# Optimization experiments

Hardware: AMD Instinct MI355X
Metric: run time of the kernel (lower is better)

## Reference

```python
import jax, jax.numpy as jnp
import numpy as np

EPS = 1e-5
NEG_SLOPE = 0.01


def setup_inputs() -> dict:
    key = jax.random.key(0)
    ks = jax.random.split(key, 5)
    B, T, I, H = 16, 16384, 64, 128
    s = 1.0 / np.sqrt(H)
    return {
        "x": jax.random.normal(ks[0], (B, T, I), dtype=jnp.float32),
        "W_ih": jax.random.normal(ks[1], (4 * H, I), dtype=jnp.float32) * s,
        "W_hh": jax.random.normal(ks[2], (4 * H, H), dtype=jnp.float32) * s,
        "b_ih": jax.random.normal(ks[3], (4 * H,), dtype=jnp.float32) * s,
        "b_hh": jax.random.normal(ks[4], (4 * H,), dtype=jnp.float32) * s,
        "gamma": jnp.ones((H,), dtype=jnp.float32),
        "beta": jnp.zeros((H,), dtype=jnp.float32),
    }


def _lstm(x, W_ih, W_hh, b_ih, b_hh):
    B, T, _ = x.shape
    H = W_hh.shape[1]
    # Precompute input contributions for all timesteps: [B, T, 4H]
    gx = jnp.einsum('bti,gi->btg', x, W_ih) + b_ih + b_hh

    def step(carry, g_t):
        h, c = carry
        g = g_t + h @ W_hh.T  # [B, 4H]
        i, f, gg, o = jnp.split(g, 4, axis=-1)  # PyTorch gate order i,f,g,o
        i = jax.nn.sigmoid(i)
        f = jax.nn.sigmoid(f)
        gg = jnp.tanh(gg)
        o = jax.nn.sigmoid(o)
        c = f * c + i * gg
        h = o * jnp.tanh(c)
        return (h, c), h

    h0 = jnp.zeros((B, H), dtype=x.dtype)
    (hn, cn), out = jax.lax.scan(step, (h0, h0), jnp.swapaxes(gx, 0, 1))
    return jnp.swapaxes(out, 0, 1), hn, cn  # out: [B, T, H]


def reference(x, W_ih, W_hh, b_ih, b_hh, gamma, beta):
    B, T, _ = x.shape
    H = W_hh.shape[1]
    out, hn, cn = _lstm(x, W_ih, W_hh, b_ih, b_hh)
    # BatchNorm1d (training mode) over flattened [B*T, H]
    flat = out.reshape(-1, H)
    mean = flat.mean(axis=0)
    var = flat.var(axis=0)  # biased variance, as PyTorch uses for normalization
    norm = (flat - mean) * jax.lax.rsqrt(var + EPS) * gamma + beta
    y = jax.nn.leaky_relu(norm.reshape(B, T, H), NEG_SLOPE)
    return (y, (hn[None], cn[None]))  # hn/cn: [num_layers=1, B, H]
```

## Files before the change

### kernel.cpp

```cpp
#include <hip/hip_runtime.h>
#include <hip/hip_bf16.h>
#include <cstdint>

#define TB 16
#define TT 16384
#define TI 64
#define TH 128
#define TG 512

typedef _Float16 half2_t __attribute__((ext_vector_type(2)));

__device__ __forceinline__ float sigf(float z) {
    return 1.0f / (1.0f + __expf(-z));
}
__device__ __forceinline__ float tanhf_fast(float z) {
    return 2.0f / (1.0f + __expf(-2.0f * z)) - 1.0f;
}
__device__ __forceinline__ float4 ld4(const float* p) {
    return *reinterpret_cast<const float4*>(p);
}
__device__ __forceinline__ void fma4(float4& acc, const float4 w, const float4 h) {
    acc.x = fmaf(w.x, h.x, acc.x);
    acc.y = fmaf(w.y, h.y, acc.y);
    acc.z = fmaf(w.z, h.z, acc.z);
    acc.w = fmaf(w.w, h.w, acc.w);
}
__device__ __forceinline__ float hsum4(const float4 a) {
    return (a.x + a.y) + (a.z + a.w);
}
__device__ __forceinline__ void pin2(half2_t& v) {
    asm volatile("" : "+v"(v));
}

__global__ __launch_bounds__(256, 2) void gx_precompute(
    const float* __restrict__ x, const float* __restrict__ W_ih,
    const float* __restrict__ b_ih, const float* __restrict__ b_hh,
    float* __restrict__ gx)
{
    const int tid  = threadIdx.x;
    const int j    = tid & (TH - 1);
    const int pair = tid >> 7;
    const int row_a = pair * 2 * TH + j;
    const int row_b = row_a + TH;

    float4 ua[TI / 4], ub[TI / 4];
#pragma unroll
    for (int k4 = 0; k4 < TI / 4; ++k4) {
        ua[k4] = ld4(W_ih + (size_t)row_a * TI + k4 * 4);
        ub[k4] = ld4(W_ih + (size_t)row_b * TI + k4 * 4);
    }
    const float bias_a = b_ih[row_a] + b_hh[row_a];
    const float bias_b = b_ih[row_b] + b_hh[row_b];

    __shared__ __align__(16) float xs[2][TI];
    const int ROWS = 128;
    const size_t r0 = (size_t)blockIdx.x * ROWS;

    if (tid < TI / 4)
        *reinterpret_cast<float4*>(&xs[0][tid * 4]) = ld4(x + r0 * TI + tid * 4);
    __syncthreads();
    float4 xreg = make_float4(0.f, 0.f, 0.f, 0.f);
    if (tid < TI / 4) xreg = ld4(x + (r0 + 1) * TI + tid * 4);

#pragma unroll 1
    for (int rr = 0; rr < ROWS; ++rr) {
        const float* xrow = xs[rr & 1];
        float4 aa = make_float4(0.f, 0.f, 0.f, 0.f);
        float4 ab = make_float4(0.f, 0.f, 0.f, 0.f);
#pragma unroll
        for (int k4 = 0; k4 < TI / 4; ++k4) {
            const float4 x4 = *reinterpret_cast<const float4*>(&xrow[k4 * 4]);
            fma4(aa, ua[k4], x4);
            fma4(ab, ub[k4], x4);
        }
        if (tid < TI / 4) {
            if (rr + 1 < ROWS)
                *reinterpret_cast<float4*>(&xs[(rr + 1) & 1][tid * 4]) = xreg;
            if (rr + 2 < ROWS) xreg = ld4(x + (r0 + rr + 2) * TI + tid * 4);
        }
        float* grow = gx + (r0 + rr) * (size_t)TG;
        grow[row_a] = hsum4(aa) + bias_a;
        grow[row_b] = hsum4(ab) + bias_b;

        asm volatile("s_waitcnt lgkmcnt(0)" ::: "memory");
        __builtin_amdgcn_s_barrier();
    }
}

__global__
__attribute__((amdgpu_flat_work_group_size(512, 512), amdgpu_waves_per_eu(2, 2)))
void lstm_scan_fp16(
    const float* __restrict__ W_hh, const float* __restrict__ gx,
    float* __restrict__ y, float* __restrict__ hn, float* __restrict__ cn)
{
    const int b    = blockIdx.x;
    const int tid  = threadIdx.x;
    const int j    = tid & (TH - 1);
    const int gate = tid >> 7;

    __shared__ __align__(16) half2_t h2_lds[TH / 2];
    __shared__ __align__(16) float   g_lds[TG];

    half2_t wh2[TH / 2];
#pragma unroll
    for (int k = 0; k < TH / 4; ++k) {
        const float4 wv = ld4(W_hh + (size_t)tid * TH + k * 4);
        wh2[2 * k]     = half2_t{(_Float16)wv.x, (_Float16)wv.y};
        wh2[2 * k + 1] = half2_t{(_Float16)wv.z, (_Float16)wv.w};
    }
#pragma unroll
    for (int k = 0; k < TH / 2; ++k) pin2(wh2[k]);

    if (tid < TH / 2) h2_lds[tid] = half2_t{(_Float16)0.f, (_Float16)0.f};
    float c_state = 0.0f;
    float h_keep  = 0.0f;

    const float* gp_base = gx + (size_t)b * TT * TG;
    float g_c  = gp_base[tid];
    float g_n1 = gp_base[TG + tid];
    float g_n2 = gp_base[2 * TG + tid];
    const float* gp = gp_base + 3 * (size_t)TG;
    float* yp = y + (size_t)b * TT * TH;

    __syncthreads();

#pragma unroll 1
    for (int t = 0; t < TT; ++t) {
        float g_n3 = 0.f;
        if (t + 3 < TT) g_n3 = gp[tid];
        gp += TG;

        float a0 = 0.f, a1 = 0.f, a2 = 0.f, a3 = 0.f;
        const float4* hv4 = reinterpret_cast<const float4*>(h2_lds);
#pragma unroll
        for (int k4 = 0; k4 < 16; ++k4) {
            const float4 hv = hv4[k4];
            const half2_t h0 = __builtin_bit_cast(half2_t, hv.x);
            const half2_t h1 = __builtin_bit_cast(half2_t, hv.y);
            const half2_t h2 = __builtin_bit_cast(half2_t, hv.z);
            const half2_t h3 = __builtin_bit_cast(half2_t, hv.w);
            a0 = __builtin_amdgcn_fdot2(wh2[4 * k4 + 0], h0, a0, false);
            a1 = __builtin_amdgcn_fdot2(wh2[4 * k4 + 1], h1, a1, false);
            a2 = __builtin_amdgcn_fdot2(wh2[4 * k4 + 2], h2, a2, false);
            a3 = __builtin_amdgcn_fdot2(wh2[4 * k4 + 3], h3, a3, false);
        }
        const float p = ((a0 + a1) + (a2 + a3)) + g_c;

        const float act = (gate == 2) ? tanhf_fast(p) : sigf(p);
        g_lds[tid] = act;

        asm volatile("s_waitcnt lgkmcnt(0)" ::: "memory");
        __builtin_amdgcn_s_barrier();

        if (tid < TH) {
            const float gi = g_lds[j];
            const float gf = g_lds[TH + j];
            const float gg = g_lds[2 * TH + j];
            const float go = g_lds[3 * TH + j];
            c_state = fmaf(gf, c_state, gi * gg);
            h_keep  = go * tanhf_fast(c_state);
            reinterpret_cast<_Float16*>(h2_lds)[j] = (_Float16)h_keep;
            yp[(size_t)t * TH + j] = h_keep;
        }

        g_c = g_n1; g_n1 = g_n2; g_n2 = g_n3;

        asm volatile("s_waitcnt lgkmcnt(0)" ::: "memory");
        __builtin_amdgcn_s_barrier();
    }

    if (tid < TH) {
        hn[(size_t)b * TH + j] = h_keep;
        cn[(size_t)b * TH + j] = c_state;
    }
}

__global__ __launch_bounds__(512, 2) void lstm_scan_fused(
    const float* __restrict__ x, const float* __restrict__ W_ih,
    const float* __restrict__ W_hh, const float* __restrict__ b_ih,
    const float* __restrict__ b_hh,
    float* __restrict__ y, float* __restrict__ hn, float* __restrict__ cn)
{
    const int b    = blockIdx.x;
    const int tid  = threadIdx.x;
    const int j    = tid & (TH - 1);
    const int gate = tid >> 7;

    __shared__ __align__(16) float h_lds[TH];
    __shared__ __align__(16) float g_lds[TG];
    __shared__ __align__(16) float xs[2][TI];

    float4 w[TH / 4];
#pragma unroll
    for (int k4 = 0; k4 < TH / 4; ++k4)
        w[k4] = ld4(W_hh + (size_t)tid * TH + k4 * 4);
    float4 u[TI / 4];
#pragma unroll
    for (int k4 = 0; k4 < TI / 4; ++k4)
        u[k4] = ld4(W_ih + (size_t)tid * TI + k4 * 4);
    const float bias = b_ih[tid] + b_hh[tid];

    if (tid < TH) h_lds[tid] = 0.0f;
    float c_state = 0.0f;
    float h_keep  = 0.0f;

    float4 xreg = make_float4(0.f, 0.f, 0.f, 0.f);
    const float* xp = x + ((size_t)b * TT + 2) * TI;
    float* yp = y + (size_t)b * TT * TH;

    if (tid < TI / 4)
        *reinterpret_cast<float4*>(&xs[0][tid * 4]) =
            ld4(x + ((size_t)b * TT + 0) * TI + tid * 4);
    __syncthreads();
    if (tid < TI / 4)
        xreg = ld4(x + ((size_t)b * TT + 1) * TI + tid * 4);

#pragma unroll 1
    for (int t = 0; t < TT; ++t) {
        float4 acc = make_float4(0.f, 0.f, 0.f, 0.f);
#pragma unroll
        for (int k4 = 0; k4 < TH / 4; ++k4) {
            const float4 h4 = *reinterpret_cast<const float4*>(&h_lds[k4 * 4]);
            fma4(acc, w[k4], h4);
        }
        float p = hsum4(acc);
        {
            float4 fx = make_float4(0.f, 0.f, 0.f, 0.f);
            const float* xrow = xs[t & 1];
#pragma unroll
            for (int k4 = 0; k4 < TI / 4; ++k4) {
                const float4 x4 = *reinterpret_cast<const float4*>(&xrow[k4 * 4]);
                fma4(fx, u[k4], x4);
            }
            p += hsum4(fx) + bias;
        }

        const float act = (gate == 2) ? tanhf_fast(p) : sigf(p);
        g_lds[tid] = act;

        asm volatile("s_waitcnt lgkmcnt(0)" ::: "memory");
        __builtin_amdgcn_s_barrier();

        if (tid < TH) {
            const float gi = g_lds[j];
            const float gf = g_lds[TH + j];
            const float gg = g_lds[2 * TH + j];
            const float go = g_lds[3 * TH + j];
            c_state = fmaf(gf, c_state, gi * gg);
            h_keep  = go * tanhf_fast(c_state);
            h_lds[j] = h_keep;
            yp[(size_t)t * TH + j] = h_keep;
        }

        if (tid < TI / 4) {
            if (t + 1 < TT)
                *reinterpret_cast<float4*>(&xs[(t + 1) & 1][tid * 4]) = xreg;
            if (t + 2 < TT) xreg = ld4(xp + tid * 4);
        }
        xp += TI;

        asm volatile("s_waitcnt lgkmcnt(0)" ::: "memory");
        __builtin_amdgcn_s_barrier();
    }

    if (tid < TH) {
        hn[(size_t)b * TH + j] = h_keep;
        cn[(size_t)b * TH + j] = c_state;
    }
}

__global__ void bn_zero(float* ws) { ws[threadIdx.x] = 0.0f; }

__global__ __launch_bounds__(256) void bn_stats(const float* __restrict__ y,
                                                float* __restrict__ ws)
{
    const int tid  = threadIdx.x;
    const int col4 = tid & 31;
    const int rg   = tid >> 5;
    const int NROW = TB * TT;
    float4 s = make_float4(0.f, 0.f, 0.f, 0.f);
    float4 q = make_float4(0.f, 0.f, 0.f, 0.f);
    for (int row = blockIdx.x * 8 + rg; row < NROW; row += gridDim.x * 8) {
        const float4 v = ld4(y + (size_t)row * TH + col4 * 4);
        s.x += v.x; s.y += v.y; s.z += v.z; s.w += v.w;
        q.x = fmaf(v.x, v.x, q.x); q.y = fmaf(v.y, v.y, q.y);
        q.z = fmaf(v.z, v.z, q.z); q.w = fmaf(v.w, v.w, q.w);
    }
    __shared__ float4 ls[256], lq[256];
    ls[tid] = s; lq[tid] = q;
    __syncthreads();
    if (tid < 32) {
        float4 S = ls[tid], Q = lq[tid];
        for (int g2 = 1; g2 < 8; ++g2) {
            const float4 a = ls[g2 * 32 + tid], b2 = lq[g2 * 32 + tid];
            S.x += a.x; S.y += a.y; S.z += a.z; S.w += a.w;
            Q.x += b2.x; Q.y += b2.y; Q.z += b2.z; Q.w += b2.w;
        }
        atomicAdd(&ws[tid * 4 + 0], S.x); atomicAdd(&ws[tid * 4 + 1], S.y);
        atomicAdd(&ws[tid * 4 + 2], S.z); atomicAdd(&ws[tid * 4 + 3], S.w);
        atomicAdd(&ws[TH + tid * 4 + 0], Q.x); atomicAdd(&ws[TH + tid * 4 + 1], Q.y);
        atomicAdd(&ws[TH + tid * 4 + 2], Q.z); atomicAdd(&ws[TH + tid * 4 + 3], Q.w);
    }
}

__global__ __launch_bounds__(256) void bn_apply(float* __restrict__ y,
                                                const float* __restrict__ ws,
                                                const float* __restrict__ gamma,
                                                const float* __restrict__ beta)
{
    const int tid  = threadIdx.x;
    const int col4 = tid & 31;
    const int rg   = tid >> 5;
    const int NROW = TB * TT;
    const float invN = 1.0f / (float)(TB * TT);

    const float4 sm = ld4(ws + col4 * 4);
    const float4 sq = ld4(ws + TH + col4 * 4);
    const float4 gm = ld4(gamma + col4 * 4);
    const float4 bt = ld4(beta + col4 * 4);
    float4 mean, scale, shift;
    mean.x = sm.x * invN; mean.y = sm.y * invN;
    mean.z = sm.z * invN; mean.w = sm.w * invN;
    scale.x = rsqrtf(fmaf(-mean.x, mean.x, sq.x * invN) + 1e-5f) * gm.x;
    scale.y = rsqrtf(fmaf(-mean.y, mean.y, sq.y * invN) + 1e-5f) * gm.y;
    scale.z = rsqrtf(fmaf(-mean.z, mean.z, sq.z * invN) + 1e-5f) * gm.z;
    scale.w = rsqrtf(fmaf(-mean.w, mean.w, sq.w * invN) + 1e-5f) * gm.w;
    shift.x = bt.x - mean.x * scale.x; shift.y = bt.y - mean.y * scale.y;
    shift.z = bt.z - mean.z * scale.z; shift.w = bt.w - mean.w * scale.w;

    for (int row = blockIdx.x * 8 + rg; row < NROW; row += gridDim.x * 8) {
        float* p = y + (size_t)row * TH + col4 * 4;
        float4 v = *reinterpret_cast<const float4*>(p);
        v.x = fmaf(v.x, scale.x, shift.x); v.y = fmaf(v.y, scale.y, shift.y);
        v.z = fmaf(v.z, scale.z, shift.z); v.w = fmaf(v.w, scale.w, shift.w);
        v.x = fmaxf(v.x, 0.01f * v.x); v.y = fmaxf(v.y, 0.01f * v.y);
        v.z = fmaxf(v.z, 0.01f * v.z); v.w = fmaxf(v.w, 0.01f * v.w);
        *reinterpret_cast<float4*>(p) = v;
    }
}

extern "C" void kernel_launch(void* const* d_in, const int* in_sizes, int n_in,
                              void* d_out, int out_size, void* d_ws, size_t ws_size,
                              hipStream_t stream)
{
    const float* x     = (const float*)d_in[0];
    const float* W_ih  = (const float*)d_in[1];
    const float* W_hh  = (const float*)d_in[2];
    const float* b_ih  = (const float*)d_in[3];
    const float* b_hh  = (const float*)d_in[4];
    const float* gamma = (const float*)d_in[5];
    const float* beta  = (const float*)d_in[6];

    float* y  = (float*)d_out;
    float* hn = y + (size_t)TB * TT * TH;
    float* cn = hn + TB * TH;

    float* ws_stats = (float*)d_ws;
    const size_t GX_BYTES = (size_t)TB * TT * TG * sizeof(float);
    const bool use_ws = ws_size >= GX_BYTES + 4096;

    bn_zero<<<1, 256, 0, stream>>>(ws_stats);

    if (use_ws) {
        float* gxbuf = (float*)((char*)d_ws + 4096);
        gx_precompute<<<2048, 256, 0, stream>>>(x, W_ih, b_ih, b_hh, gxbuf);
        lstm_scan_fp16<<<TB, 512, 0, stream>>>(W_hh, gxbuf, y, hn, cn);
    } else {
        lstm_scan_fused<<<TB, 512, 0, stream>>>(x, W_ih, W_hh, b_ih, b_hh,
                                                y, hn, cn);
    }

    bn_stats<<<512, 256, 0, stream>>>(y, ws_stats);
    bn_apply<<<2048, 256, 0, stream>>>(y, ws_stats, gamma, beta);
}
```

Before: 10.75 ms.

## Split each hidden unit's K-reduction across four lanes to remove a barrier per step

Reorganizes the recurrent scan so four adjacent lanes each compute partial dot products for all four gates of one hidden unit over a quarter of K. The partials are combined with xor shuffles, so every lane holds all the gate pre-activations. This removes the gate-exchange LDS round trip and one of the two block barriers per timestep. The hidden state is double-buffered in LDS so a single barrier per step is enough. The gx load is split across the four lanes via selector multipliers, and the activation math is now done redundantly in all four lanes.

Measured after the change: 13.35 ms. +24.2%, slower.

```diff
diff --git a/kernel.cpp b/kernel.cpp
--- a/kernel.cpp
+++ b/kernel.cpp
@@ -89,90 +89,115 @@
 
 __global__
 __attribute__((amdgpu_flat_work_group_size(512, 512), amdgpu_waves_per_eu(2, 2)))
-void lstm_scan_fp16(
+void lstm_scan_quad(
     const float* __restrict__ W_hh, const float* __restrict__ gx,
     float* __restrict__ y, float* __restrict__ hn, float* __restrict__ cn)
 {
-    const int b    = blockIdx.x;
-    const int tid  = threadIdx.x;
-    const int j    = tid & (TH - 1);
-    const int gate = tid >> 7;
-
-    __shared__ __align__(16) half2_t h2_lds[TH / 2];
-    __shared__ __align__(16) float   g_lds[TG];
-
-    half2_t wh2[TH / 2];
-#pragma unroll
-    for (int k = 0; k < TH / 4; ++k) {
-        const float4 wv = ld4(W_hh + (size_t)tid * TH + k * 4);
-        wh2[2 * k]     = half2_t{(_Float16)wv.x, (_Float16)wv.y};
-        wh2[2 * k + 1] = half2_t{(_Float16)wv.z, (_Float16)wv.w};
-    }
-#pragma unroll
-    for (int k = 0; k < TH / 2; ++k) pin2(wh2[k]);
-
-    if (tid < TH / 2) h2_lds[tid] = half2_t{(_Float16)0.f, (_Float16)0.f};
+    const int b   = blockIdx.x;
+    const int tid = threadIdx.x;
+    const int j   = tid >> 2;
+    const int q   = tid & 3;
+
+    __shared__ __align__(16) half2_t h2[2][TH / 2];
+
+    half2_t w[4][16];
+#pragma unroll
+    for (int s = 0; s < 4; ++s) {
+        const float* wr = W_hh + (size_t)(s * TH + j) * TH + q * 32;
+#pragma unroll
+        for (int k4 = 0; k4 < 8; ++k4) {
+            const float4 v = ld4(wr + k4 * 4);
+            w[s][2 * k4]     = half2_t{(_Float16)v.x, (_Float16)v.y};
+            w[s][2 * k4 + 1] = half2_t{(_Float16)v.z, (_Float16)v.w};
+        }
+    }
+#pragma unroll
+    for (int s = 0; s < 4; ++s)
+#pragma unroll
+        for (int k = 0; k < 16; ++k) pin2(w[s][k]);
+
+    const float sel0 = (q == 0) ? 1.f : 0.f;
+    const float sel1 = (q == 1) ? 1.f : 0.f;
+    const float sel2 = (q == 2) ? 1.f : 0.f;
+    const float sel3 = (q == 3) ? 1.f : 0.f;
+
+    if (tid < TH / 2) h2[0][tid] = half2_t{(_Float16)0.f, (_Float16)0.f};
     float c_state = 0.0f;
     float h_keep  = 0.0f;
 
-    const float* gp_base = gx + (size_t)b * TT * TG;
-    float g_c  = gp_base[tid];
-    float g_n1 = gp_base[TG + tid];
-    float g_n2 = gp_base[2 * TG + tid];
-    const float* gp = gp_base + 3 * (size_t)TG;
+    const float* gp = gx + (size_t)b * TT * TG + (q * TH + j);
+    float g_c  = gp[0];
+    float g_n1 = gp[TG];
+    float g_n2 = gp[2 * (size_t)TG];
     float* yp = y + (size_t)b * TT * TH;
 
     __syncthreads();
 
+    int cur = 0;
 #pragma unroll 1
     for (int t = 0; t < TT; ++t) {
         float g_n3 = 0.f;
-        if (t + 3 < TT) g_n3 = gp[tid];
-        gp += TG;
-
-        float a0 = 0.f, a1 = 0.f, a2 = 0.f, a3 = 0.f;
-        const float4* hv4 = reinterpret_cast<const float4*>(h2_lds);
-#pragma unroll
-        for (int k4 = 0; k4 < 16; ++k4) {
-            const float4 hv = hv4[k4];
-            const half2_t h0 = __builtin_bit_cast(half2_t, hv.x);
-            const half2_t h1 = __builtin_bit_cast(half2_t, hv.y);
-            const half2_t h2 = __builtin_bit_cast(half2_t, hv.z);
-            const half2_t h3 = __builtin_bit_cast(half2_t, hv.w);
-            a0 = __builtin_amdgcn_fdot2(wh2[4 * k4 + 0], h0, a0, false);
-            a1 = __builtin_amdgcn_fdot2(wh2[4 * k4 + 1], h1, a1, false);
-            a2 = __builtin_amdgcn_fdot2(wh2[4 * k4 + 2], h2, a2, false);
-            a3 = __builtin_amdgcn_fdot2(wh2[4 * k4 + 3], h3, a3, false);
-        }
-        const float p = ((a0 + a1) + (a2 + a3)) + g_c;
-
-        const float act = (gate == 2) ? tanhf_fast(p) : sigf(p);
-        g_lds[tid] = act;
+        if (t + 3 < TT) g_n3 = gp[(size_t)(t + 3) * TG];
+
+        const float4* hv4 = reinterpret_cast<const float4*>(&h2[cur][q * 16]);
+        const float4 hA = hv4[0], hB = hv4[1], hC = hv4[2], hD = hv4[3];
+        half2_t hh[16];
+        hh[0]  = __builtin_bit_cast(half2_t, hA.x);
+        hh[1]  = __builtin_bit_cast(half2_t, hA.y);
+        hh[2]  = __builtin_bit_cast(half2_t, hA.z);
+        hh[3]  = __builtin_bit_cast(half2_t, hA.w);
+        hh[4]  = __builtin_bit_cast(half2_t, hB.x);
+        hh[5]  = __builtin_bit_cast(half2_t, hB.y);
+        hh[6]  = __builtin_bit_cast(half2_t, hB.z);
+        hh[7]  = __builtin_bit_cast(half2_t, hB.w);
+        hh[8]  = __builtin_bit_cast(half2_t, hC.x);
+        hh[9]  = __builtin_bit_cast(half2_t, hC.y);
+        hh[10] = __builtin_bit_cast(half2_t, hC.z);
+        hh[11] = __builtin_bit_cast(half2_t, hC.w);
+        hh[12] = __builtin_bit_cast(half2_t, hD.x);
+        hh[13] = __builtin_bit_cast(half2_t, hD.y);
+        hh[14] = __builtin_bit_cast(half2_t, hD.z);
+        hh[15] = __builtin_bit_cast(half2_t, hD.w);
+
+        float p0 = sel0 * g_c;
+        float p1 = sel1 * g_c;
+        float p2 = sel2 * g_c;
+        float p3 = sel3 * g_c;
+#pragma unroll
+        for (int k = 0; k < 16; ++k) {
+            p0 = __builtin_amdgcn_fdot2(w[0][k], hh[k], p0, false);
+            p1 = __builtin_amdgcn_fdot2(w[1][k], hh[k], p1, false);
+            p2 = __builtin_amdgcn_fdot2(w[2][k], hh[k], p2, false);
+            p3 = __builtin_amdgcn_fdot2(w[3][k], hh[k], p3, false);
+        }
+
+        p0 += __shfl_xor(p0, 1); p1 += __shfl_xor(p1, 1);
+        p2 += __shfl_xor(p2, 1); p3 += __shfl_xor(p3, 1);
+        p0 += __shfl_xor(p0, 2); p1 += __shfl_xor(p1, 2);
+        p2 += __shfl_xor(p2, 2); p3 += __shfl_xor(p3, 2);
+
+        const float gi = sigf(p0);
+        const float gf = sigf(p1);
+        const float gg = tanhf_fast(p2);
+        const float go = sigf(p3);
+        c_state = fmaf(gf, c_state, gi * gg);
+        h_keep  = go * tanhf_fast(c_state);
+
+        const int nxt = cur ^ 1;
+        if (q == 0)
+            reinterpret_cast<_Float16*>(&h2[nxt][0])[j] = (_Float16)h_keep;
+        if (q == 1)
+            yp[(size_t)t * TH + j] = h_keep;
+
+        g_c = g_n1; g_n1 = g_n2; g_n2 = g_n3;
+        cur = nxt;
 
         asm volatile("s_waitcnt lgkmcnt(0)" ::: "memory");
         __builtin_amdgcn_s_barrier();
-
-        if (tid < TH) {
-            const float gi = g_lds[j];
-            const float gf = g_lds[TH + j];
-            const float gg = g_lds[2 * TH + j];
-            const float go = g_lds[3 * TH + j];
-            c_state = fmaf(gf, c_state, gi * gg);
-            h_keep  = go * tanhf_fast(c_state);
-            reinterpret_cast<_Float16*>(h2_lds)[j] = (_Float16)h_keep;
-            yp[(size_t)t * TH + j] = h_keep;
-        }
-
-        g_c = g_n1; g_n1 = g_n2; g_n2 = g_n3;
-
-        asm volatile("s_waitcnt lgkmcnt(0)" ::: "memory");
-        __builtin_amdgcn_s_barrier();
-    }
-
-    if (tid < TH) {
-        hn[(size_t)b * TH + j] = h_keep;
-        cn[(size_t)b * TH + j] = c_state;
-    }
+    }
+
+    if (q == 2) hn[(size_t)b * TH + j] = h_keep;
+    if (q == 3) cn[(size_t)b * TH + j] = c_state;
 }
 
 __global__ __launch_bounds__(512, 2) void lstm_scan_fused(
@@ -364,7 +389,7 @@
     if (use_ws) {
         float* gxbuf = (float*)((char*)d_ws + 4096);
         gx_precompute<<<2048, 256, 0, stream>>>(x, W_ih, b_ih, b_hh, gxbuf);
-        lstm_scan_fp16<<<TB, 512, 0, stream>>>(W_hh, gxbuf, y, hn, cn);
+        lstm_scan_quad<<<TB, 512, 0, stream>>>(W_hh, gxbuf, y, hn, cn);
     } else {
         lstm_scan_fused<<<TB, 512, 0, stream>>>(x, W_ih, W_hh, b_ih, b_hh,
                                                 y, hn, cn);
```
